# Performance work log

Measured on AMD Instinct MI355X. Metric: run time of the kernel, lower is better.

Reference implementation:

```python
import jax, jax.numpy as jnp
import numpy as np
import math

B, S, D, H, M = 2, 2048, 1024, 16, 64
HD = D // H  # head_dim = 64


def setup_inputs() -> dict:
    key = jax.random.key(0)
    ks = jax.random.split(key, 16)
    inp = {
        "query": jax.random.normal(ks[0], (B, S, D), jnp.float32),
        "key": jax.random.normal(ks[1], (B, S, D), jnp.float32),
        "value": jax.random.normal(ks[2], (B, S, D), jnp.float32),
        "mask": jax.random.randint(ks[3], (B, 1, 1, S), 0, 2, jnp.int32),
        "Wq": jax.random.normal(ks[4], (D, D), jnp.float32) * 0.02,
        "bq": jnp.zeros((D,), jnp.float32),
        "Wk": jax.random.normal(ks[5], (D, D), jnp.float32) * 0.02,
        "bk": jnp.zeros((D,), jnp.float32),
        "Wv": jax.random.normal(ks[6], (D, D), jnp.float32) * 0.02,
        "bv": jnp.zeros((D,), jnp.float32),
        "Wo": jax.random.normal(ks[7], (D, D), jnp.float32) * 0.02,
        "bo": jnp.zeros((D,), jnp.float32),
        "m_k": jax.random.normal(ks[8], (1, M, D), jnp.float32) * (1.0 / HD),
        "m_v": jax.random.normal(ks[9], (1, M, D), jnp.float32) * (1.0 / M),
    }
    return inp


def reference(query, key, value, mask, Wq, bq, Wk, bk, Wv, bv, Wo, bo, m_k, m_v):
    b, nq, d = query.shape
    nk = key.shape[1]
    h, hd, m = H, HD, M
    scale = math.sqrt(hd)

    Q = query @ Wq.T + bq                      # [b, nq, d]
    K = key @ Wk.T + bk                        # [b, nk, d]
    V = value @ Wv.T + bv                      # [b, nk, d]

    mk = scale * jnp.broadcast_to(m_k, (b, m, d))           # sqrt(head_dim)*m_k
    mv = math.sqrt(m) * jnp.broadcast_to(m_v, (b, m, d))    # sqrt(m)*m_v

    K = jnp.concatenate([K, mk], axis=1)       # [b, nk+m, d]
    V = jnp.concatenate([V, mv], axis=1)

    Qh = Q.reshape(b, nq, h, hd).transpose(0, 2, 1, 3)           # [b,h,nq,hd]
    Kh = K.reshape(b, nk + m, h, hd).transpose(0, 2, 1, 3)       # [b,h,nk+m,hd]
    Vh = V.reshape(b, nk + m, h, hd).transpose(0, 2, 1, 3)

    energy = jnp.einsum('bhqd,bhkd->bhqk', Qh, Kh) / scale       # [b,h,nq,nk+m]
    # mask only the first nk key columns; memory slots are never masked
    masked = jnp.where(mask == 0, jnp.float32(-1e20), energy[..., :nk])
    energy = jnp.concatenate([masked, energy[..., nk:]], axis=-1)

    attention = jax.nn.softmax(energy, axis=-1)
    x = jnp.einsum('bhqk,bhkd->bhqd', attention, Vh)             # [b,h,nq,hd]
    x = x.transpose(0, 2, 1, 3).reshape(b, nq, d)
    return x @ Wo.T + bo
```

## Files before the change

kernel.cpp:

```cpp
#include <hip/hip_runtime.h>
#include <hip/hip_bf16.h>
#include <stdint.h>

#define B_  2
#define S_  2048
#define D_  1024
#define H_  16
#define HD_ 64
#define M_  64
#define SKM (S_ + M_)
#define LOG2E 1.44269504088896340736f

typedef __attribute__((ext_vector_type(8))) short s16x8;
typedef __attribute__((ext_vector_type(4))) float f32x4;
typedef __attribute__((ext_vector_type(16))) float f32x16;

#define GLOAD16(gp, lp) __builtin_amdgcn_global_load_lds( \
    (const __attribute__((address_space(1))) void*)(gp),  \
    (__attribute__((address_space(3))) void*)(lp), 16, 0, 0)

#define WAITVM(N) do { asm volatile("s_waitcnt vmcnt(" #N ")" ::: "memory"); \
                       __builtin_amdgcn_sched_barrier(0); } while (0)
#define BARRIER() do { asm volatile("" ::: "memory"); \
                       __builtin_amdgcn_s_barrier(); \
                       asm volatile("" ::: "memory"); } while (0)

__device__ __forceinline__ unsigned short f2bf(float f) {
  union { float f; unsigned int u; } v; v.f = f;
  unsigned int r = v.u + 0x7fffu + ((v.u >> 16) & 1u);
  return (unsigned short)(r >> 16);
}

__device__ __forceinline__ unsigned pkbf(float lo, float hi) {
  union { __hip_bfloat162 b; unsigned u; } t;
  t.b = __float22bfloat162_rn(make_float2(lo, hi));
  return t.u;
}

__global__ void compact_mask(const int* __restrict__ mask,
                             int* __restrict__ idx, int* __restrict__ cnt) {
  const int b = blockIdx.x;
  __shared__ int base, wsum[4];
  if (threadIdx.x == 0) base = 0;
  const int lane = threadIdx.x & 63, w = threadIdx.x >> 6;
  __syncthreads();
  for (int c = 0; c < S_; c += 256) {
    int key = c + threadIdx.x;
    int mv = mask[b * S_ + key];
    unsigned long long bal = __ballot(mv != 0);
    int pre = __popcll(bal & ((1ull << lane) - 1ull));
    if (lane == 0) wsum[w] = __popcll(bal);
    __syncthreads();
    int woff = 0;
    for (int i = 0; i < w; i++) woff += wsum[i];
    int tot = wsum[0] + wsum[1] + wsum[2] + wsum[3];
    if (mv) idx[b * S_ + base + woff + pre] = key;
    __syncthreads();
    if (threadIdx.x == 0) base += tot;
    __syncthreads();
  }
  if (threadIdx.x == 0) cnt[b] = base;
}

__global__ void cvt_fused(const float* __restrict__ q,
                          const float* __restrict__ w0, const float* __restrict__ w1,
                          const float* __restrict__ w2, const float* __restrict__ w3,
                          const float* __restrict__ key, const float* __restrict__ value,
                          unsigned short* __restrict__ qf,
                          unsigned short* __restrict__ o0, unsigned short* __restrict__ o1,
                          unsigned short* __restrict__ o2, unsigned short* __restrict__ o3,
                          unsigned short* __restrict__ kf, unsigned short* __restrict__ vf,
                          const int* __restrict__ idx, const int* __restrict__ cnt) {
  const size_t NQs = (size_t)B_ * S_ * D_;
  if (blockIdx.x < 8192) {
    size_t i = ((size_t)blockIdx.x * 256 + threadIdx.x) * 4;
    const float* in; unsigned short* out; size_t off;
    if (i < NQs) { in = q; out = qf; off = i; }
    else {
      size_t j = i - NQs;
      int wsel = (int)(j >> 20);
      off = j & ((1u << 20) - 1);
      in  = (wsel == 0) ? w0 : (wsel == 1) ? w1 : (wsel == 2) ? w2 : w3;
      out = (wsel == 0) ? o0 : (wsel == 1) ? o1 : (wsel == 2) ? o2 : o3;
    }
    float4 v = *(const float4*)&in[off];
    ushort4 o;
    o.x = f2bf(v.x); o.y = f2bf(v.y); o.z = f2bf(v.z); o.w = f2bf(v.w);
    *(ushort4*)&out[off] = o;
  } else {
    int gid = blockIdx.x - 8192;
    int kv = gid >> 12, rem = gid & 4095;
    int b = rem >> 11, j = rem & 2047;
    if (j >= cnt[b]) return;
    const float* in = kv ? value : key;
    unsigned short* out = kv ? vf : kf;
    int src = idx[b * S_ + j];
    const float* ip = in + ((size_t)(b * S_) + src) * D_;
    unsigned short* op = out + ((size_t)(b * S_) + j) * D_;
    int t = threadIdx.x * 4;
    float4 v = *(const float4*)&ip[t];
    ushort4 o;
    o.x = f2bf(v.x); o.y = f2bf(v.y); o.z = f2bf(v.z); o.w = f2bf(v.w);
    *(ushort4*)&op[t] = o;
  }
}

__global__ void fill_mem(const float* __restrict__ mk, const float* __restrict__ mv,
                         unsigned short* __restrict__ Kb, unsigned short* __restrict__ VtG,
                         const int* __restrict__ cnt) {
  int i = blockIdx.x * 256 + threadIdx.x;
  int row = i >> 10, col = i & 1023;
  int hI = col >> 6, dd = col & 63;
  unsigned short kv = f2bf(8.0f * mk[i]);
  unsigned short vv = f2bf(8.0f * mv[i]);
#pragma unroll
  for (int b = 0; b < B_; b++) {
    int c = cnt[b];
    Kb[((size_t)(b * SKM) + c + row) * D_ + col] = kv;
    VtG[((size_t)(b * H_ + hI) * HD_ + dd) * SKM + c + row] = vv;
  }
}

__device__ __forceinline__ void gemm_core64(
    const unsigned short* __restrict__ A,
    const unsigned short* __restrict__ Bw,
    unsigned short* As, unsigned short* Bs,
    int mBase, int nBase,
    int tid, f32x4 acc[4][2]) {
  const int lane = tid & 63, w = tid >> 6;
  const int wr = w >> 2, wc = w & 3;
  const int lr = lane & 15, lk = lane >> 4;
  const int rg = lane >> 3;
  const int sr0 = w * 8 + rg;
  const int ca = (lane & 7) ^ (rg & 7);
  const int NT = D_ / 64;

#define STAGE_(buf, k0)                                                          \
  {                                                                              \
    GLOAD16(&A[(size_t)(mBase + sr0) * D_ + (k0) + ca * 8],                      \
            &As[(buf) * (128 * 64) + (w * 8) * 64]);                             \
    GLOAD16(&A[(size_t)(mBase + 64 + sr0) * D_ + (k0) + ca * 8],                 \
            &As[(buf) * (128 * 64) + (64 + w * 8) * 64]);                        \
    GLOAD16(&Bw[(size_t)(nBase + sr0) * D_ + (k0) + ca * 8],                     \
            &Bs[(buf) * (128 * 64) + (w * 8) * 64]);                             \
    GLOAD16(&Bw[(size_t)(nBase + 64 + sr0) * D_ + (k0) + ca * 8],                \
            &Bs[(buf) * (128 * 64) + (64 + w * 8) * 64]);                        \
  }

  STAGE_(0, 0);
  int cur = 0;
  for (int t = 0; t < NT; ++t) {
    if (t + 1 < NT) {
      STAGE_(cur ^ 1, (t + 1) * 64);
      WAITVM(4);
    } else {
      WAITVM(0);
    }
    BARRIER();
#pragma unroll
    for (int ks = 0; ks < 2; ks++) {
      s16x8 af[4], bf[2];
#pragma unroll
      for (int mi = 0; mi < 4; mi++) {
        int row = wr * 64 + mi * 16 + lr;
        af[mi] = *(const s16x8*)&As[cur * (128 * 64) + row * 64 + (((ks * 4 + lk) ^ (row & 7)) << 3)];
      }
#pragma unroll
      for (int ni = 0; ni < 2; ni++) {
        int row = wc * 32 + ni * 16 + lr;
        bf[ni] = *(const s16x8*)&Bs[cur * (128 * 64) + row * 64 + (((ks * 4 + lk) ^ (row & 7)) << 3)];
      }
#pragma unroll
      for (int mi = 0; mi < 4; mi++)
#pragma unroll
        for (int ni = 0; ni < 2; ni++)
          acc[mi][ni] = __builtin_amdgcn_mfma_f32_16x16x32_bf16(af[mi], bf[ni], acc[mi][ni], 0, 0, 0);
    }
    BARRIER();
    cur ^= 1;
  }
#undef STAGE_
}

__global__ __launch_bounds__(512)
void gemm_qkv(const unsigned short* __restrict__ qf, const unsigned short* __restrict__ kf,
              const unsigned short* __restrict__ vf,
              const unsigned short* __restrict__ wq, const unsigned short* __restrict__ wk,
              const unsigned short* __restrict__ wv,
              const float* __restrict__ bq, const float* __restrict__ bk,
              const float* __restrict__ bv,
              unsigned short* __restrict__ Qb, unsigned short* __restrict__ Kb,
              unsigned short* __restrict__ Vt,
              const int* __restrict__ cnt) {
  __shared__ __align__(16) unsigned short As[2 * 128 * 64];
  __shared__ __align__(16) unsigned short Bs[2 * 128 * 64];
  const int z = blockIdx.x >> 8;
  const int local = blockIdx.x & 255;
  const int wsz = (local & 7) * 32 + (local >> 3);
  const int nBase = (wsz & 7) * 128, mBase = (wsz >> 3) * 128;
  const int bb = (mBase >= S_);
  if (z) {
    if (mBase - bb * S_ >= cnt[bb]) return;
  }
  const unsigned short* A  = (z == 0) ? qf : (z == 1) ? kf : vf;
  const unsigned short* Bw = (z == 0) ? wq : (z == 1) ? wk : wv;
  const float* bias        = (z == 0) ? bq : (z == 1) ? bk : bv;

  const int tid = threadIdx.x, lane = tid & 63;
  const int w = tid >> 6, wr = w >> 2, wc = w & 3;
  const int lr = lane & 15, lk = lane >> 4;

  const f32x4 fz = {0.f, 0.f, 0.f, 0.f};
  f32x4 acc[4][2];
#pragma unroll
  for (int i = 0; i < 4; i++)
#pragma unroll
    for (int j = 0; j < 2; j++) acc[i][j] = fz;

  gemm_core64(A, Bw, As, Bs, mBase, nBase, tid, acc);

  const float alpha = (z == 0) ? 0.125f * LOG2E : 1.0f;
#pragma unroll
  for (int mi = 0; mi < 4; mi++)
#pragma unroll
    for (int ni = 0; ni < 2; ni++)
#pragma unroll
      for (int r = 0; r < 4; r++) {
        int gr = mBase + wr * 64 + mi * 16 + lk * 4 + r;
        int gc = nBase + wc * 32 + ni * 16 + lr;
        float v = (acc[mi][ni][r] + bias[gc]) * alpha;
        if (z == 2) {
          int s = gr - bb * S_;
          int hI = gc >> 6, dd = gc & 63;
          Vt[((size_t)(bb * H_ + hI) * HD_ + dd) * SKM + s] = f2bf(v);
        } else if (z == 1) {
          int orow = gr + bb * M_;
          Kb[(size_t)orow * D_ + gc] = f2bf(v);
        } else {
          Qb[(size_t)gr * D_ + gc] = f2bf(v);
        }
      }
}

__global__ __launch_bounds__(512)
void gemm_o(const unsigned short* __restrict__ A, const unsigned short* __restrict__ Bw,
            const float* __restrict__ bias, float* __restrict__ Cout) {
  __shared__ __align__(16) unsigned short As[2 * 128 * 64];
  __shared__ __align__(16) unsigned short Bs[2 * 128 * 64];
  const int local = blockIdx.x & 255;
  const int wsz = (local & 7) * 32 + (local >> 3);
  const int nBase = (wsz & 7) * 128, mBase = (wsz >> 3) * 128;
  const int tid = threadIdx.x, lane = tid & 63;
  const int w = tid >> 6, wr = w >> 2, wc = w & 3;
  const int lr = lane & 15, lk = lane >> 4;

  const f32x4 fz = {0.f, 0.f, 0.f, 0.f};
  f32x4 acc[4][2];
#pragma unroll
  for (int i = 0; i < 4; i++)
#pragma unroll
    for (int j = 0; j < 2; j++) acc[i][j] = fz;

  gemm_core64(A, Bw, As, Bs, mBase, nBase, tid, acc);

#pragma unroll
  for (int mi = 0; mi < 4; mi++)
#pragma unroll
    for (int ni = 0; ni < 2; ni++)
#pragma unroll
      for (int r = 0; r < 4; r++) {
        int gr = mBase + wr * 64 + mi * 16 + lk * 4 + r;
        int gc = nBase + wc * 32 + ni * 16 + lr;
        Cout[(size_t)gr * D_ + gc] = acc[mi][ni][r] + bias[gc];
      }
}

__global__ __launch_bounds__(512)
void attn_kernel(const unsigned short* __restrict__ Qb,
                 const unsigned short* __restrict__ Kb,
                 const unsigned short* __restrict__ VtG,
                 const int* __restrict__ cnt,
                 unsigned short* __restrict__ Xb) {
  __shared__ __align__(16) unsigned short Ks[2 * 64 * 64];
  __shared__ __align__(16) unsigned short Vs[2 * 64 * 64];

  const int tid = threadIdx.x, lane = tid & 63, w = tid >> 6;
  const int l31 = lane & 31, hh = lane >> 5;
  const int qt = blockIdx.x, h = blockIdx.y, b = blockIdx.z;

  const int total = cnt[b] + M_;
  const int nt = (total + 63) >> 6;

  const int r0 = tid >> 3, c0 = tid & 7;
  const int ck = c0 ^ (r0 & 7);
  const unsigned short* Kg = Kb + (size_t)b * SKM * D_ + (size_t)h * HD_;
  const unsigned short* Vg = VtG + (size_t)(b * H_ + h) * HD_ * SKM;

  const unsigned short* qp = Qb + ((size_t)(b * S_) + qt * 256 + w * 32 + l31) * D_ + h * HD_;
  s16x8 qf[4];
#pragma unroll
  for (int ds = 0; ds < 4; ds++) qf[ds] = *(const s16x8*)&qp[ds * 16 + hh * 8];

  f32x16 accO[2];
#pragma unroll
  for (int dt = 0; dt < 2; dt++)
#pragma unroll
    for (int j = 0; j < 16; j++) accO[dt][j] = 0.f;
  float m_r = -1e20f, l_r = 0.f;

  uint4 kr0, vr0;
  auto LOAD = [&](int kt) {
    kr0 = *(const uint4*)&Kg[(size_t)(kt * 64 + r0) * D_ + c0 * 8];
    vr0 = *(const uint4*)&Vg[(size_t)r0 * SKM + kt * 64 + c0 * 8];
  };

  LOAD(0);
  *(uint4*)&Ks[r0 * 64 + ck * 8] = kr0;
  *(uint4*)&Vs[r0 * 64 + ck * 8] = vr0;
  __syncthreads();
  int cur = 0;

  for (int kt = 0; kt < nt; ++kt) {
    const bool pre = (kt + 1 < nt);
    if (pre) LOAD(kt + 1);

    const unsigned short* Kc = &Ks[cur * 4096];
    const unsigned short* Vc = &Vs[cur * 4096];
    f32x16 p0, p1;
#pragma unroll
    for (int j = 0; j < 16; j++) { p0[j] = 0.f; p1[j] = 0.f; }
    __builtin_amdgcn_s_setprio(1);
#pragma unroll
    for (int ds = 0; ds < 4; ds++) {
      s16x8 ka0 = *(const s16x8*)&Kc[l31 * 64 + (((ds * 2 + hh) ^ (l31 & 7)) << 3)];
      s16x8 ka1 = *(const s16x8*)&Kc[(32 + l31) * 64 + (((ds * 2 + hh) ^ (l31 & 7)) << 3)];
      p0 = __builtin_amdgcn_mfma_f32_32x32x16_bf16(ka0, qf[ds], p0, 0, 0, 0);
      p1 = __builtin_amdgcn_mfma_f32_32x32x16_bf16(ka1, qf[ds], p1, 0, 0, 0);
    }
    __builtin_amdgcn_s_setprio(0);

    if (kt == nt - 1) {
      int valid = total - kt * 64;
#pragma unroll
      for (int j = 0; j < 16; j++) {
        int kl = (j & 3) + 8 * (j >> 2) + 4 * hh;
        if (kl >= valid) p0[j] = -1e30f;
        if (kl + 32 >= valid) p1[j] = -1e30f;
      }
    }

    float vmax = fmaxf(p0[0], p1[0]);
#pragma unroll
    for (int j = 1; j < 16; j++) vmax = fmaxf(vmax, fmaxf(p0[j], p1[j]));
    vmax = fmaxf(vmax, __shfl_xor(vmax, 32));
    if (!__all(vmax - m_r <= 8.0f)) {
      float mnew = fmaxf(m_r, vmax);
      float fac = __builtin_amdgcn_exp2f(m_r - mnew);
      m_r = mnew;
      l_r *= fac;
#pragma unroll
      for (int dt = 0; dt < 2; dt++)
#pragma unroll
        for (int j = 0; j < 16; j++) accO[dt][j] *= fac;
    }
    float sum = 0.f;
#pragma unroll
    for (int j = 0; j < 16; j++) {
      p0[j] = __builtin_amdgcn_exp2f(p0[j] - m_r); sum += p0[j];
      p1[j] = __builtin_amdgcn_exp2f(p1[j] - m_r); sum += p1[j];
    }
    sum += __shfl_xor(sum, 32);
    l_r += sum;

    s16x8 pf_[4];
#pragma unroll
    for (int ks = 0; ks < 4; ks++) {
      const int base = (ks & 1) * 8;
#define ELT(t) ((ks >= 2) ? p1[base + (t)] : p0[base + (t)])
      unsigned w0 = pkbf(ELT(0), ELT(1));
      unsigned w1 = pkbf(ELT(2), ELT(3));
      unsigned w2 = pkbf(ELT(4), ELT(5));
      unsigned w3 = pkbf(ELT(6), ELT(7));
#undef ELT
      unsigned s0 = hh ? w0 : w2;
      unsigned s1 = hh ? w1 : w3;
      unsigned g0 = (unsigned)__shfl_xor((int)s0, 32);
      unsigned g1 = (unsigned)__shfl_xor((int)s1, 32);
      union { s16x8 v; unsigned u[4]; } pf;
      pf.u[0] = hh ? g0 : w0;
      pf.u[1] = hh ? g1 : w1;
      pf.u[2] = hh ? w2 : g0;
      pf.u[3] = hh ? w3 : g1;
      pf_[ks] = pf.v;
    }

    __builtin_amdgcn_s_setprio(1);
#pragma unroll
    for (int dt = 0; dt < 2; dt++)
#pragma unroll
      for (int ks = 0; ks < 4; ks++) {
        s16x8 va = *(const s16x8*)&Vc[(dt * 32 + l31) * 64 + (((ks * 2 + hh) ^ (l31 & 7)) << 3)];
        accO[dt] = __builtin_amdgcn_mfma_f32_32x32x16_bf16(va, pf_[ks], accO[dt], 0, 0, 0);
      }
    __builtin_amdgcn_s_setprio(0);

    if (pre) {
      *(uint4*)&Ks[(cur ^ 1) * 4096 + r0 * 64 + ck * 8] = kr0;
      *(uint4*)&Vs[(cur ^ 1) * 4096 + r0 * 64 + ck * 8] = vr0;
      __syncthreads();
      cur ^= 1;
    }
  }

  float invl = 1.0f / l_r;
  size_t orow = ((size_t)(b * S_) + qt * 256 + w * 32 + l31) * D_ + h * HD_;
#pragma unroll
  for (int dt = 0; dt < 2; dt++)
#pragma unroll
    for (int j = 0; j < 16; j++) {
      int d = dt * 32 + (j & 3) + 8 * (j >> 2) + 4 * hh;
      Xb[orow + d] = f2bf(accO[dt][j] * invl);
    }
}

extern "C" void kernel_launch(void* const* d_in, const int* in_sizes, int n_in,
                              void* d_out, int out_size, void* d_ws, size_t ws_size,
                              hipStream_t stream) {
  const float* query = (const float*)d_in[0];
  const float* key   = (const float*)d_in[1];
  const float* value = (const float*)d_in[2];
  const int*   mask  = (const int*)d_in[3];
  const float* Wq    = (const float*)d_in[4];
  const float* bq    = (const float*)d_in[5];
  const float* Wk    = (const float*)d_in[6];
  const float* bk    = (const float*)d_in[7];
  const float* Wv    = (const float*)d_in[8];
  const float* bv    = (const float*)d_in[9];
  const float* Wo    = (const float*)d_in[10];
  const float* bo    = (const float*)d_in[11];
  const float* m_k   = (const float*)d_in[12];
  const float* m_v   = (const float*)d_in[13];

  const int NQ = B_ * S_ * D_;
  const int NW = D_ * D_;
  const int NK = B_ * SKM * D_;

  unsigned short* ws = (unsigned short*)d_ws;
  unsigned short* qf = ws;
  unsigned short* kf = qf + NQ;
  unsigned short* vf = kf + NQ;
  unsigned short* wq = vf + NQ;
  unsigned short* wk = wq + NW;
  unsigned short* wv = wk + NW;
  unsigned short* wo = wv + NW;
  unsigned short* Qb = wo + NW;
  unsigned short* Kb = Qb + NQ;
  unsigned short* Vt = Kb + NK;
  unsigned short* Xb = Vt + NK;
  int* idx = (int*)(Xb + NQ);
  int* cnt = idx + B_ * S_;

  compact_mask<<<B_, 256, 0, stream>>>(mask, idx, cnt);
  cvt_fused<<<16384, 256, 0, stream>>>(query, Wq, Wk, Wv, Wo, key, value,
                                       qf, wq, wk, wv, wo, kf, vf, idx, cnt);

  gemm_qkv<<<768, 512, 0, stream>>>(qf, kf, vf, wq, wk, wv, bq, bk, bv, Qb, Kb, Vt, cnt);
  fill_mem<<<(M_ * D_) / 256, 256, 0, stream>>>(m_k, m_v, Kb, Vt, cnt);

  attn_kernel<<<dim3(S_ / 256, H_, B_), 512, 0, stream>>>(Qb, Kb, Vt, cnt, Xb);

  gemm_o<<<256, 512, 0, stream>>>(Xb, wo, bo, (float*)d_out);
}
```

Before: 122.9 us.

## Process two KV tiles per barrier in attention and widen mask compaction

```diff
diff --git a/kernel.cpp b/kernel.cpp
--- a/kernel.cpp
+++ b/kernel.cpp
@@ -40,11 +40,11 @@
 __global__ void compact_mask(const int* __restrict__ mask,
                              int* __restrict__ idx, int* __restrict__ cnt) {
   const int b = blockIdx.x;
-  __shared__ int base, wsum[4];
+  __shared__ int base, wsum[16];
   if (threadIdx.x == 0) base = 0;
   const int lane = threadIdx.x & 63, w = threadIdx.x >> 6;
   __syncthreads();
-  for (int c = 0; c < S_; c += 256) {
+  for (int c = 0; c < S_; c += 1024) {
     int key = c + threadIdx.x;
     int mv = mask[b * S_ + key];
     unsigned long long bal = __ballot(mv != 0);
@@ -52,8 +52,11 @@
     if (lane == 0) wsum[w] = __popcll(bal);
     __syncthreads();
     int woff = 0;
-    for (int i = 0; i < w; i++) woff += wsum[i];
-    int tot = wsum[0] + wsum[1] + wsum[2] + wsum[3];
+#pragma unroll
+    for (int i = 0; i < 16; i++) woff += (i < w) ? wsum[i] : 0;
+    int tot = 0;
+#pragma unroll
+    for (int i = 0; i < 16; i++) tot += wsum[i];
     if (mv) idx[b * S_ + base + woff + pre] = key;
     __syncthreads();
     if (threadIdx.x == 0) base += tot;
@@ -281,8 +284,8 @@
                  const unsigned short* __restrict__ VtG,
                  const int* __restrict__ cnt,
                  unsigned short* __restrict__ Xb) {
-  __shared__ __align__(16) unsigned short Ks[2 * 64 * 64];
-  __shared__ __align__(16) unsigned short Vs[2 * 64 * 64];
+  __shared__ __align__(16) unsigned short Ks[2 * 2 * 64 * 64];
+  __shared__ __align__(16) unsigned short Vs[2 * 2 * 64 * 64];
 
   const int tid = threadIdx.x, lane = tid & 63, w = tid >> 6;
   const int l31 = lane & 31, hh = lane >> 5;
@@ -290,6 +293,7 @@
 
   const int total = cnt[b] + M_;
   const int nt = (total + 63) >> 6;
+  const int npair = (nt + 1) >> 1;
 
   const int r0 = tid >> 3, c0 = tid & 7;
   const int ck = c0 ^ (r0 & 7);
@@ -308,105 +312,120 @@
     for (int j = 0; j < 16; j++) accO[dt][j] = 0.f;
   float m_r = -1e20f, l_r = 0.f;
 
-  uint4 kr0, vr0;
-  auto LOAD = [&](int kt) {
-    kr0 = *(const uint4*)&Kg[(size_t)(kt * 64 + r0) * D_ + c0 * 8];
-    vr0 = *(const uint4*)&Vg[(size_t)r0 * SKM + kt * 64 + c0 * 8];
+  uint4 kr0, kr1, vr0, vr1;
+  auto LOAD = [&](int pair) {
+    int t0 = pair * 2;     if (t0 > nt - 1) t0 = nt - 1;
+    int t1 = pair * 2 + 1; if (t1 > nt - 1) t1 = nt - 1;
+    kr0 = *(const uint4*)&Kg[(size_t)(t0 * 64 + r0) * D_ + c0 * 8];
+    kr1 = *(const uint4*)&Kg[(size_t)(t1 * 64 + r0) * D_ + c0 * 8];
+    vr0 = *(const uint4*)&Vg[(size_t)r0 * SKM + t0 * 64 + c0 * 8];
+    vr1 = *(const uint4*)&Vg[(size_t)r0 * SKM + t1 * 64 + c0 * 8];
   };
 
   LOAD(0);
   *(uint4*)&Ks[r0 * 64 + ck * 8] = kr0;
+  *(uint4*)&Ks[4096 + r0 * 64 + ck * 8] = kr1;
   *(uint4*)&Vs[r0 * 64 + ck * 8] = vr0;
+  *(uint4*)&Vs[4096 + r0 * 64 + ck * 8] = vr1;
   __syncthreads();
   int cur = 0;
 
-  for (int kt = 0; kt < nt; ++kt) {
-    const bool pre = (kt + 1 < nt);
-    if (pre) LOAD(kt + 1);
-
-    const unsigned short* Kc = &Ks[cur * 4096];
-    const unsigned short* Vc = &Vs[cur * 4096];
-    f32x16 p0, p1;
-#pragma unroll
-    for (int j = 0; j < 16; j++) { p0[j] = 0.f; p1[j] = 0.f; }
-    __builtin_amdgcn_s_setprio(1);
-#pragma unroll
-    for (int ds = 0; ds < 4; ds++) {
-      s16x8 ka0 = *(const s16x8*)&Kc[l31 * 64 + (((ds * 2 + hh) ^ (l31 & 7)) << 3)];
-      s16x8 ka1 = *(const s16x8*)&Kc[(32 + l31) * 64 + (((ds * 2 + hh) ^ (l31 & 7)) << 3)];
-      p0 = __builtin_amdgcn_mfma_f32_32x32x16_bf16(ka0, qf[ds], p0, 0, 0, 0);
-      p1 = __builtin_amdgcn_mfma_f32_32x32x16_bf16(ka1, qf[ds], p1, 0, 0, 0);
-    }
-    __builtin_amdgcn_s_setprio(0);
-
-    if (kt == nt - 1) {
-      int valid = total - kt * 64;
+  for (int p = 0; p < npair; ++p) {
+    const bool pre = (p + 1 < npair);
+    if (pre) LOAD(p + 1);
+
+#pragma unroll
+    for (int s = 0; s < 2; s++) {
+      const int kt = p * 2 + s;
+      if (kt >= nt) break;
+      const unsigned short* Kc = &Ks[cur * 8192 + s * 4096];
+      const unsigned short* Vc = &Vs[cur * 8192 + s * 4096];
+
+      f32x16 p0, p1;
+#pragma unroll
+      for (int j = 0; j < 16; j++) { p0[j] = 0.f; p1[j] = 0.f; }
+      __builtin_amdgcn_s_setprio(1);
+#pragma unroll
+      for (int ds = 0; ds < 4; ds++) {
+        s16x8 ka0 = *(const s16x8*)&Kc[l31 * 64 + (((ds * 2 + hh) ^ (l31 & 7)) << 3)];
+        s16x8 ka1 = *(const s16x8*)&Kc[(32 + l31) * 64 + (((ds * 2 + hh) ^ (l31 & 7)) << 3)];
+        p0 = __builtin_amdgcn_mfma_f32_32x32x16_bf16(ka0, qf[ds], p0, 0, 0, 0);
+        p1 = __builtin_amdgcn_mfma_f32_32x32x16_bf16(ka1, qf[ds], p1, 0, 0, 0);
+      }
+      __builtin_amdgcn_s_setprio(0);
+
+      if (kt == nt - 1) {
+        int valid = total - kt * 64;
+#pragma unroll
+        for (int j = 0; j < 16; j++) {
+          int kl = (j & 3) + 8 * (j >> 2) + 4 * hh;
+          if (kl >= valid) p0[j] = -1e30f;
+          if (kl + 32 >= valid) p1[j] = -1e30f;
+        }
+      }
+
+      float vmax = fmaxf(p0[0], p1[0]);
+#pragma unroll
+      for (int j = 1; j < 16; j++) vmax = fmaxf(vmax, fmaxf(p0[j], p1[j]));
+      vmax = fmaxf(vmax, __shfl_xor(vmax, 32));
+      if (!__all(vmax - m_r <= 8.0f)) {
+        float mnew = fmaxf(m_r, vmax);
+        float fac = __builtin_amdgcn_exp2f(m_r - mnew);
+        m_r = mnew;
+        l_r *= fac;
+#pragma unroll
+        for (int dt = 0; dt < 2; dt++)
+#pragma unroll
+          for (int j = 0; j < 16; j++) accO[dt][j] *= fac;
+      }
+      float sum = 0.f;
 #pragma unroll
       for (int j = 0; j < 16; j++) {
-        int kl = (j & 3) + 8 * (j >> 2) + 4 * hh;
-        if (kl >= valid) p0[j] = -1e30f;
-        if (kl + 32 >= valid) p1[j] = -1e30f;
-      }
-    }
-
-    float vmax = fmaxf(p0[0], p1[0]);
-#pragma unroll
-    for (int j = 1; j < 16; j++) vmax = fmaxf(vmax, fmaxf(p0[j], p1[j]));
-    vmax = fmaxf(vmax, __shfl_xor(vmax, 32));
-    if (!__all(vmax - m_r <= 8.0f)) {
-      float mnew = fmaxf(m_r, vmax);
-      float fac = __builtin_amdgcn_exp2f(m_r - mnew);
-      m_r = mnew;
-      l_r *= fac;
+        p0[j] = __builtin_amdgcn_exp2f(p0[j] - m_r); sum += p0[j];
+        p1[j] = __builtin_amdgcn_exp2f(p1[j] - m_r); sum += p1[j];
+      }
+      sum += __shfl_xor(sum, 32);
+      l_r += sum;
+
+      s16x8 pf_[4];
+#pragma unroll
+      for (int ks = 0; ks < 4; ks++) {
+        const int base = (ks & 1) * 8;
+#define ELT(t) ((ks >= 2) ? p1[base + (t)] : p0[base + (t)])
+        unsigned w0 = pkbf(ELT(0), ELT(1));
+        unsigned w1 = pkbf(ELT(2), ELT(3));
+        unsigned w2 = pkbf(ELT(4), ELT(5));
+        unsigned w3 = pkbf(ELT(6), ELT(7));
+#undef ELT
+        unsigned s0 = hh ? w0 : w2;
+        unsigned s1 = hh ? w1 : w3;
+        unsigned g0 = (unsigned)__shfl_xor((int)s0, 32);
+        unsigned g1 = (unsigned)__shfl_xor((int)s1, 32);
+        union { s16x8 v; unsigned u[4]; } pf;
+        pf.u[0] = hh ? g0 : w0;
+        pf.u[1] = hh ? g1 : w1;
+        pf.u[2] = hh ? w2 : g0;
+        pf.u[3] = hh ? w3 : g1;
+        pf_[ks] = pf.v;
+      }
+
+      __builtin_amdgcn_s_setprio(1);
 #pragma unroll
       for (int dt = 0; dt < 2; dt++)
 #pragma unroll
-        for (int j = 0; j < 16; j++) accO[dt][j] *= fac;
-    }
-    float sum = 0.f;
-#pragma unroll
-    for (int j = 0; j < 16; j++) {
-      p0[j] = __builtin_amdgcn_exp2f(p0[j] - m_r); sum += p0[j];
-      p1[j] = __builtin_amdgcn_exp2f(p1[j] - m_r); sum += p1[j];
-    }
-    sum += __shfl_xor(sum, 32);
-    l_r += sum;
-
-    s16x8 pf_[4];
-#pragma unroll
-    for (int ks = 0; ks < 4; ks++) {
-      const int base = (ks & 1) * 8;
-#define ELT(t) ((ks >= 2) ? p1[base + (t)] : p0[base + (t)])
-      unsigned w0 = pkbf(ELT(0), ELT(1));
-      unsigned w1 = pkbf(ELT(2), ELT(3));
-      unsigned w2 = pkbf(ELT(4), ELT(5));
-      unsigned w3 = pkbf(ELT(6), ELT(7));
-#undef ELT
-      unsigned s0 = hh ? w0 : w2;
-      unsigned s1 = hh ? w1 : w3;
-      unsigned g0 = (unsigned)__shfl_xor((int)s0, 32);
-      unsigned g1 = (unsigned)__shfl_xor((int)s1, 32);
-      union { s16x8 v; unsigned u[4]; } pf;
-      pf.u[0] = hh ? g0 : w0;
-      pf.u[1] = hh ? g1 : w1;
-      pf.u[2] = hh ? w2 : g0;
-      pf.u[3] = hh ? w3 : g1;
-      pf_[ks] = pf.v;
-    }
-
-    __builtin_amdgcn_s_setprio(1);
-#pragma unroll
-    for (int dt = 0; dt < 2; dt++)
-#pragma unroll
-      for (int ks = 0; ks < 4; ks++) {
-        s16x8 va = *(const s16x8*)&Vc[(dt * 32 + l31) * 64 + (((ks * 2 + hh) ^ (l31 & 7)) << 3)];
-        accO[dt] = __builtin_amdgcn_mfma_f32_32x32x16_bf16(va, pf_[ks], accO[dt], 0, 0, 0);
-      }
-    __builtin_amdgcn_s_setprio(0);
+        for (int ks = 0; ks < 4; ks++) {
+          s16x8 va = *(const s16x8*)&Vc[(dt * 32 + l31) * 64 + (((ks * 2 + hh) ^ (l31 & 7)) << 3)];
+          accO[dt] = __builtin_amdgcn_mfma_f32_32x32x16_bf16(va, pf_[ks], accO[dt], 0, 0, 0);
+        }
+      __builtin_amdgcn_s_setprio(0);
+    }
 
     if (pre) {
-      *(uint4*)&Ks[(cur ^ 1) * 4096 + r0 * 64 + ck * 8] = kr0;
-      *(uint4*)&Vs[(cur ^ 1) * 4096 + r0 * 64 + ck * 8] = vr0;
+      int ob = (cur ^ 1) * 8192;
+      *(uint4*)&Ks[ob + r0 * 64 + ck * 8] = kr0;
+      *(uint4*)&Ks[ob + 4096 + r0 * 64 + ck * 8] = kr1;
+      *(uint4*)&Vs[ob + r0 * 64 + ck * 8] = vr0;
+      *(uint4*)&Vs[ob + 4096 + r0 * 64 + ck * 8] = vr1;
       __syncthreads();
       cur ^= 1;
     }
@@ -460,7 +479,7 @@
   int* idx = (int*)(Xb + NQ);
   int* cnt = idx + B_ * S_;
 
-  compact_mask<<<B_, 256, 0, stream>>>(mask, idx, cnt);
+  compact_mask<<<B_, 1024, 0, stream>>>(mask, idx, cnt);
   cvt_fused<<<16384, 256, 0, stream>>>(query, Wq, Wk, Wv, Wo, key, value,
                                        qf, wq, wk, wv, wo, kf, vf, idx, cnt);
 
```

Result: no change. 122.4 us (-0.4%).
